# Optimization experiments

Hardware: AMD Instinct MI355X
Metric: run time of the kernel (lower is better)

The kernel has to match this reference:

```python
import jax, jax.numpy as jnp
import numpy as np

DIM = 768
H = 12
D = DIM // H  # head_dim = 64
SCALE = D ** -0.5


def _split_heads(x):
    # [b, n, h*d] -> [b, h, n, d]
    b, n, _ = x.shape
    return x.reshape(b, n, H, D).transpose(0, 2, 1, 3)


def setup_inputs() -> dict:
    key = jax.random.key(0)
    ks = jax.random.split(key, 16)
    B, NQ, NKV = 2, 2048, 2048
    w_init = lambda k: jax.random.normal(k, (DIM, DIM), dtype=jnp.float32) * 0.02
    return {
        "words": jax.random.normal(ks[0], (B, NQ, DIM), dtype=jnp.float32),
        "position_words": jax.random.normal(ks[1], (B, NQ, DIM), dtype=jnp.float32),
        "conscious_words": jax.random.normal(ks[2], (B, NQ, DIM), dtype=jnp.float32),
        "cross_kv": jax.random.normal(ks[3], (B, NKV, DIM), dtype=jnp.float32),
        "position_cross": jax.random.normal(ks[4], (B, NKV, DIM), dtype=jnp.float32),
        "Wq_w": w_init(ks[5]), "Wk_w": w_init(ks[6]), "Wv_w": w_init(ks[7]),
        "Wq_p": w_init(ks[8]), "Wk_p": w_init(ks[9]),
        "Wq_c": w_init(ks[10]), "Wk_c": w_init(ks[11]),
        "latent_k": jax.random.normal(ks[12], (DIM,), dtype=jnp.float32),
        "Wo": w_init(ks[13]),
        "bo": jnp.zeros((DIM,), dtype=jnp.float32),
    }


def reference(words, position_words, conscious_words, cross_kv, position_cross,
              Wq_w, Wk_w, Wv_w, Wq_p, Wk_p, Wq_c, Wk_c, latent_k, Wo, bo):
    # Queries from three sources. Sum of the 9 pairwise QK^T scores equals
    # (sum of Qs) @ (sum of Ks)^T by bilinearity of matmul (same math as source).
    q = _split_heads(words @ Wq_w) + _split_heads(position_words @ Wq_p) \
        + _split_heads(conscious_words @ Wq_c)        # [b,h,nq,d]
    # latent conscious key: same vector for every kv position
    kc = (latent_k @ Wk_c).reshape(H, D)              # [h,d]
    k = _split_heads(cross_kv @ Wk_w) + _split_heads(position_cross @ Wk_p) \
        + kc[None, :, None, :]                        # [b,h,nkv,d]
    v = _split_heads(cross_kv @ Wv_w)                 # [b,h,nkv,d]

    score = jnp.einsum('bhid,bhjd->bhij', q, k) * SCALE  # [b,h,nq,nkv]
    attn = jax.nn.softmax(score, axis=-1)
    out = jnp.einsum('bhij,bhjd->bhid', attn, v)      # [b,h,nq,d]
    b, _, nq, _ = out.shape
    out = out.transpose(0, 2, 1, 3).reshape(b, nq, H * D)
    return out @ Wo + bo
```

## Files before the change

kernel.cpp:

```cpp
#include <hip/hip_runtime.h>
#include <math.h>

#define DIM  768
#define NH   12
#define HD   64
#define NQ   2048
#define NKV  2048
#define QSC_LOG2E 0.18033688011112042f

typedef short bf16x8  __attribute__((ext_vector_type(8)));
typedef float f32x4   __attribute__((ext_vector_type(4)));
typedef float f32x16  __attribute__((ext_vector_type(16)));

__device__ __forceinline__ unsigned short f2bf(float f) {
    unsigned u = __float_as_uint(f);
    unsigned r = (u + 0x7FFFu + ((u >> 16) & 1u)) >> 16;
    return (unsigned short)r;
}

__device__ __forceinline__ unsigned cvtpk_bf16(float a, float b) {
    unsigned r;
    asm("v_cvt_pk_bf16_f32 %0, %1, %2" : "=v"(r) : "v"(a), "v"(b));
    return r;
}

__device__ __forceinline__ void plswap(unsigned& a, unsigned& b) {
    asm("v_permlane32_swap_b32 %0, %1" : "+v"(a), "+v"(b));
}

__device__ __forceinline__ float vexp2f(float x) {
#if __has_builtin(__builtin_amdgcn_exp2f)
    return __builtin_amdgcn_exp2f(x);
#else
    float r;
    asm("v_exp_f32 %0, %1\ns_nop 0" : "=v"(r) : "v"(x));
    return r;
#endif
}

__device__ __forceinline__ void ld_lds16(void* lds, const void* g) {
    __builtin_amdgcn_global_load_lds(
        (const __attribute__((address_space(1))) unsigned int*)g,
        (__attribute__((address_space(3))) unsigned int*)lds, 16, 0, 0);
}

__device__ __forceinline__ f32x16 z16() {
    f32x16 r;
    #pragma unroll
    for (int e = 0; e < 16; ++e) r[e] = 0.f;
    return r;
}

union PB16 { unsigned u[4]; bf16x8 v; };

__global__ __launch_bounds__(256)
void kc2_kernel(const float* __restrict__ latent, const float* __restrict__ Wkc,
                float* __restrict__ kc) {
    __shared__ float red[16][17];
    int tx = threadIdx.x & 15, ty = threadIdx.x >> 4;
    int j = blockIdx.x * 16 + tx;
    float acc = 0.f;
    for (int i = ty * 48; i < ty * 48 + 48; ++i) acc += latent[i] * Wkc[i * DIM + j];
    red[ty][tx] = acc;
    __syncthreads();
    if (ty == 0) {
        float s = 0.f;
        #pragma unroll
        for (int k = 0; k < 16; ++k) s += red[k][tx];
        kc[j] = s;
    }
}

__global__ __launch_bounds__(256)
void convert_acts(const float* __restrict__ s0, const float* __restrict__ s1,
                  const float* __restrict__ s2, const float* __restrict__ s3,
                  const float* __restrict__ s4,
                  unsigned short* __restrict__ dstA, unsigned short* __restrict__ dstB) {
    const float* srcs[5] = {s0, s1, s2, s3, s4};
    int y = blockIdx.y;
    const float* s = srcs[y];
    unsigned short* d = (y < 4) ? (dstA + (size_t)y * 3145728) : dstB;
    size_t i = ((size_t)blockIdx.x * 256 + threadIdx.x) * 4;
    float4 v = *(const float4*)(s + i);
    ushort4 o;
    o.x = f2bf(v.x); o.y = f2bf(v.y); o.z = f2bf(v.z); o.w = f2bf(v.w);
    *(ushort4*)(d + i) = o;
}

__global__ __launch_bounds__(256)
void conv_w(const float* __restrict__ w0, const float* __restrict__ w1,
            const float* __restrict__ w2, const float* __restrict__ w3,
            const float* __restrict__ w4, const float* __restrict__ w5,
            const float* __restrict__ w6, unsigned short* __restrict__ dst) {
    __shared__ float t[32][33];
    const float* Ws[7] = {w0, w1, w2, w3, w4, w5, w6};
    const float* W = Ws[blockIdx.z];
    unsigned short* D = dst + (size_t)blockIdx.z * (768 * 768);
    int r0 = blockIdx.y * 32, c0 = blockIdx.x * 32;
    int tx = threadIdx.x & 31, ty = threadIdx.x >> 5;
    #pragma unroll
    for (int yy = 0; yy < 4; ++yy)
        t[ty * 4 + yy][tx] = W[(size_t)(r0 + ty * 4 + yy) * 768 + c0 + tx];
    __syncthreads();
    #pragma unroll
    for (int yy = 0; yy < 4; ++yy)
        D[(size_t)(c0 + ty * 4 + yy) * 768 + r0 + tx] = f2bf(t[tx][ty * 4 + yy]);
}

template<int NPAIR, int MODE>
__global__ __launch_bounds__(256)
void mfma_gemm(const unsigned short* __restrict__ A0, const unsigned short* __restrict__ B0,
               const unsigned short* __restrict__ A1, const unsigned short* __restrict__ B1,
               const unsigned short* __restrict__ A2, const unsigned short* __restrict__ B2,
               const float* __restrict__ bias, float scale, void* __restrict__ Cout) {
    __shared__ unsigned short As[2][64 * 64];
    __shared__ unsigned short Bs[2][128 * 64];
    const int tid = threadIdx.x;
    const int w = tid >> 6, l = tid & 63, g = l >> 4, r16 = l & 15;

    int o_lin = blockIdx.x + 6 * blockIdx.y;
    int wl = (o_lin & 7) * 48 + (o_lin >> 3);
    int bx = wl % 6, by = wl / 6;
    const int n0 = bx * 128, m0 = by * 64;

    const unsigned short* Alist[3] = {A0, A1, A2};
    const unsigned short* Blist[3] = {B0, B1, B2};

    f32x4 acc[4][2];
    #pragma unroll
    for (int i = 0; i < 4; ++i)
        #pragma unroll
        for (int j = 0; j < 2; ++j) acc[i][j] = (f32x4){0.f, 0.f, 0.f, 0.f};

#define GSTAGE(BUFI, AP, BP, K0) { \
    _Pragma("unroll") \
    for (int is = 0; is < 2; ++is) { \
        int u = is * 256 + tid, r = u >> 3, cc = u & 7; \
        int col = ((cc ^ (r & 7)) << 3); \
        ld_lds16((char*)As[BUFI] + is * 4096 + w * 1024, \
                 (AP) + (size_t)(m0 + r) * 768 + (K0) + col); } \
    _Pragma("unroll") \
    for (int is = 0; is < 4; ++is) { \
        int u = is * 256 + tid, r = u >> 3, cc = u & 7; \
        int col = ((cc ^ (r & 7)) << 3); \
        ld_lds16((char*)Bs[BUFI] + is * 4096 + w * 1024, \
                 (BP) + (size_t)(n0 + r) * 768 + (K0) + col); } }

    const int NSTEPS = NPAIR * 12;
    int pn = 0, kn = 0;
    GSTAGE(0, Alist[0], Blist[0], 0);
    kn = 64; if (kn == 768) { kn = 0; ++pn; }
    __syncthreads();

    #pragma unroll 1
    for (int st = 0; st < NSTEPS; ++st) {
        int cur = st & 1;
        if (st + 1 < NSTEPS) {
            GSTAGE(cur ^ 1, Alist[pn], Blist[pn], kn);
            kn += 64; if (kn == 768) { kn = 0; ++pn; }
        }
        const char* Ab = (const char*)As[cur];
        const char* Bb = (const char*)Bs[cur];
        #pragma unroll
        for (int kk = 0; kk < 2; ++kk) {
            bf16x8 af[4], bf[2];
            #pragma unroll
            for (int i = 0; i < 4; ++i) {
                int row = i * 16 + r16;
                af[i] = *(const bf16x8*)(Ab + row * 128 +
                          ((kk * 64 + g * 16) ^ ((row & 7) << 4)));
            }
            #pragma unroll
            for (int j = 0; j < 2; ++j) {
                int row = w * 32 + j * 16 + r16;
                bf[j] = *(const bf16x8*)(Bb + row * 128 +
                          ((kk * 64 + g * 16) ^ ((row & 7) << 4)));
            }
            #pragma unroll
            for (int i = 0; i < 4; ++i)
                #pragma unroll
                for (int j = 0; j < 2; ++j)
                    acc[i][j] = __builtin_amdgcn_mfma_f32_16x16x32_bf16(
                        af[i], bf[j], acc[i][j], 0, 0, 0);
        }
        __syncthreads();
    }
#undef GSTAGE

    #pragma unroll
    for (int i = 0; i < 4; ++i) {
        #pragma unroll
        for (int j = 0; j < 2; ++j) {
            int col = n0 + w * 32 + j * 16 + r16;
            float bv = ((MODE == 0 && bias) || MODE == 1) ? bias[col] : 0.f;
            #pragma unroll
            for (int rr = 0; rr < 4; ++rr) {
                int row = m0 + i * 16 + g * 4 + rr;
                float v = acc[i][j][rr];
                if (MODE == 2) v *= scale;
                v += bv;
                if (MODE == 1) {
                    ((float*)Cout)[(size_t)row * 768 + col] = v;
                } else if (MODE == 3) {
                    int bb = row >> 11, q = row & 2047;
                    ((unsigned short*)Cout)[(size_t)(bb * 768 + col) * 2048 + q] = f2bf(v);
                } else {
                    ((unsigned short*)Cout)[(size_t)row * 768 + col] = f2bf(v);
                }
            }
        }
    }
}

__global__ __launch_bounds__(256)
void flash2(const unsigned short* __restrict__ Qb,
            const unsigned short* __restrict__ Kb,
            const unsigned short* __restrict__ Vt,
            unsigned short* __restrict__ AO) {
    __shared__ unsigned short KV[2][2][4096];
    const int tid = threadIdx.x;
    const int w = tid >> 6, l = tid & 63, lo = l & 31, hi = l >> 5;

    int o_lin = blockIdx.x + 16 * blockIdx.y;
    int wl = (o_lin & 7) * 48 + (o_lin >> 3);
    int qi = wl & 15, bh = wl >> 4;
    int b = bh / NH, h = bh % NH;
    int q0 = qi * 128;

    bf16x8 qf[4];
    {
        const unsigned short* Qrow =
            Qb + (size_t)(b * NQ + q0 + w * 32 + lo) * DIM + h * HD + hi * 8;
        #pragma unroll
        for (int kc = 0; kc < 4; ++kc) qf[kc] = *(const bf16x8*)(Qrow + kc * 16);
    }

    f32x16 o0 = z16(), o1 = z16();
    float m = -3.0e38f, lsum = 0.f;

    const unsigned short* Kbase = Kb + (size_t)(b * NKV) * DIM + h * HD;
    const unsigned short* Vbase = Vt + ((size_t)b * DIM + h * HD) * NKV;

#define FSTAGE(BUFI, T0) { \
    _Pragma("unroll") \
    for (int is = 0; is < 2; ++is) { \
        int u = is * 256 + tid, r = u >> 3, cc = u & 7; \
        int col = ((cc ^ (r & 7)) << 3); \
        ld_lds16((char*)KV[BUFI][0] + is * 4096 + w * 1024, \
                 Kbase + (size_t)((T0) + r) * 768 + col); \
        ld_lds16((char*)KV[BUFI][1] + is * 4096 + w * 1024, \
                 Vbase + (size_t)r * 2048 + (T0) + col); } }

    FSTAGE(0, 0);
    __syncthreads();

    #pragma unroll 1
    for (int t = 0; t < 32; ++t) {
        int cur = t & 1;
        if (t < 31) FSTAGE(cur ^ 1, (t + 1) * 64);

        const char* Kp = (const char*)KV[cur][0];
        const char* Vp = (const char*)KV[cur][1];

        f32x16 s0 = z16(), s1 = z16();
        #pragma unroll
        for (int kc = 0; kc < 4; ++kc) {
            int r0 = lo, r1 = 32 + lo;
            bf16x8 k0 = *(const bf16x8*)(Kp + r0 * 128 +
                          ((kc * 32 + hi * 16) ^ ((r0 & 7) << 4)));
            bf16x8 k1 = *(const bf16x8*)(Kp + r1 * 128 +
                          ((kc * 32 + hi * 16) ^ ((r1 & 7) << 4)));
            s0 = __builtin_amdgcn_mfma_f32_32x32x16_bf16(k0, qf[kc], s0, 0, 0, 0);
            s1 = __builtin_amdgcn_mfma_f32_32x32x16_bf16(k1, qf[kc], s1, 0, 0, 0);
        }

        float a8[8];
        #pragma unroll
        for (int e = 0; e < 8; ++e)
            a8[e] = fmaxf(fmaxf(s0[e], s0[e + 8]), fmaxf(s1[e], s1[e + 8]));
        #pragma unroll
        for (int e = 0; e < 4; ++e) a8[e] = fmaxf(a8[e], a8[e + 4]);
        float pm = fmaxf(fmaxf(a8[0], a8[1]), fmaxf(a8[2], a8[3]));
        pm = fmaxf(pm, __shfl_xor(pm, 32));

        if (__any(pm > m + 10.f)) {
            float mn = fmaxf(m, pm);
            float sc = vexp2f(m - mn);
            lsum *= sc;
            #pragma unroll
            for (int e = 0; e < 16; ++e) { o0[e] *= sc; o1[e] *= sc; }
            m = mn;
        }

        #pragma unroll
        for (int e = 0; e < 16; ++e) {
            s0[e] = vexp2f(s0[e] - m);
            s1[e] = vexp2f(s1[e] - m);
        }

        float b8[8];
        #pragma unroll
        for (int e = 0; e < 8; ++e)
            b8[e] = (s0[e] + s0[e + 8]) + (s1[e] + s1[e + 8]);
        float rs = ((b8[0] + b8[1]) + (b8[2] + b8[3])) +
                   ((b8[4] + b8[5]) + (b8[6] + b8[7]));
        rs += __shfl_xor(rs, 32);
        lsum += rs;

        PB16 pb[4];
        #pragma unroll
        for (int cc = 0; cc < 2; ++cc) {
            unsigned a0 = cvtpk_bf16(s0[cc * 8 + 0], s0[cc * 8 + 1]);
            unsigned a1 = cvtpk_bf16(s0[cc * 8 + 2], s0[cc * 8 + 3]);
            unsigned b0 = cvtpk_bf16(s0[cc * 8 + 4], s0[cc * 8 + 5]);
            unsigned b1 = cvtpk_bf16(s0[cc * 8 + 6], s0[cc * 8 + 7]);
            plswap(a0, b0);
            plswap(a1, b1);
            pb[cc].u[0] = a0; pb[cc].u[1] = a1; pb[cc].u[2] = b0; pb[cc].u[3] = b1;
            unsigned c0 = cvtpk_bf16(s1[cc * 8 + 0], s1[cc * 8 + 1]);
            unsigned c1 = cvtpk_bf16(s1[cc * 8 + 2], s1[cc * 8 + 3]);
            unsigned d0 = cvtpk_bf16(s1[cc * 8 + 4], s1[cc * 8 + 5]);
            unsigned d1 = cvtpk_bf16(s1[cc * 8 + 6], s1[cc * 8 + 7]);
            plswap(c0, d0);
            plswap(c1, d1);
            pb[2 + cc].u[0] = c0; pb[2 + cc].u[1] = c1;
            pb[2 + cc].u[2] = d0; pb[2 + cc].u[3] = d1;
        }

        #pragma unroll
        for (int c = 0; c < 4; ++c) {
            int r0 = lo, r1 = 32 + lo;
            bf16x8 v0 = *(const bf16x8*)(Vp + r0 * 128 +
                          ((c * 32 + hi * 16) ^ ((r0 & 7) << 4)));
            bf16x8 v1 = *(const bf16x8*)(Vp + r1 * 128 +
                          ((c * 32 + hi * 16) ^ ((r1 & 7) << 4)));
            o0 = __builtin_amdgcn_mfma_f32_32x32x16_bf16(v0, pb[c].v, o0, 0, 0, 0);
            o1 = __builtin_amdgcn_mfma_f32_32x32x16_bf16(v1, pb[c].v, o1, 0, 0, 0);
        }
        __syncthreads();
    }
#undef FSTAGE

    float inv = 1.f / lsum;
    char* eb = (char*)KV + w * 4096;
    #pragma unroll
    for (int r = 0; r < 16; r += 2) {
        int d0 = (r & 3) + 8 * (r >> 2) + 4 * hi;
        *(unsigned*)(eb + lo * 128 + ((2 * d0) ^ ((lo & 7) << 4))) =
            cvtpk_bf16(o0[r] * inv, o0[r + 1] * inv);
        int d1 = 32 + d0;
        *(unsigned*)(eb + lo * 128 + ((2 * d1) ^ ((lo & 7) << 4))) =
            cvtpk_bf16(o1[r] * inv, o1[r + 1] * inv);
    }
    int q2 = l >> 1, h2 = l & 1;
    size_t grow = (size_t)(b * NQ + q0 + w * 32 + q2) * DIM + h * HD + h2 * 32;
    #pragma unroll
    for (int c = 0; c < 4; ++c) {
        uint4 vv = *(const uint4*)(eb + q2 * 128 + ((h2 * 64 + c * 16) ^ ((q2 & 7) << 4)));
        *(uint4*)(AO + grow + c * 8) = vv;
    }
}

extern "C" void kernel_launch(void* const* d_in, const int* in_sizes, int n_in,
                              void* d_out, int out_size, void* d_ws, size_t ws_size,
                              hipStream_t stream) {
    const float* words   = (const float*)d_in[0];
    const float* posw    = (const float*)d_in[1];
    const float* consc   = (const float*)d_in[2];
    const float* cross   = (const float*)d_in[3];
    const float* pcross  = (const float*)d_in[4];
    const float* Wq_w    = (const float*)d_in[5];
    const float* Wk_w    = (const float*)d_in[6];
    const float* Wv_w    = (const float*)d_in[7];
    const float* Wq_p    = (const float*)d_in[8];
    const float* Wk_p    = (const float*)d_in[9];
    const float* Wq_c    = (const float*)d_in[10];
    const float* Wk_c    = (const float*)d_in[11];
    const float* latentk = (const float*)d_in[12];
    const float* Wo      = (const float*)d_in[13];
    const float* bo      = (const float*)d_in[14];

    char* arena = (char*)d_ws;
    const size_t ACTB = 6291456;
    unsigned short* act0 = (unsigned short*)(arena);
    unsigned short* act1 = (unsigned short*)(arena + ACTB);
    unsigned short* act2 = (unsigned short*)(arena + 2 * ACTB);
    unsigned short* act3 = (unsigned short*)(arena + 3 * ACTB);
    unsigned short* wt   = (unsigned short*)(arena + 4 * ACTB);
    const size_t WTE = 768 * 768;
    unsigned short* qb  = (unsigned short*)(arena + 4 * ACTB + 7 * WTE * 2);
    unsigned short* pcb = (unsigned short*)((char*)qb + ACTB);
    float* kcv          = (float*)((char*)pcb + ACTB);

    unsigned short* kb = act1;
    unsigned short* vt = act2;
    unsigned short* ao = act0;

    convert_acts<<<dim3(3072, 5), dim3(256), 0, stream>>>(
        words, posw, consc, cross, pcross, act0, pcb);
    conv_w<<<dim3(24, 24, 7), dim3(256), 0, stream>>>(
        Wq_w, Wq_p, Wq_c, Wk_w, Wk_p, Wv_w, Wo, wt);
    kc2_kernel<<<dim3(48), dim3(256), 0, stream>>>(latentk, Wk_c, kcv);

    mfma_gemm<3, 2><<<dim3(6, 64), dim3(256), 0, stream>>>(
        act0, wt + 0 * WTE, act1, wt + 1 * WTE, act2, wt + 2 * WTE,
        nullptr, QSC_LOG2E, qb);
    mfma_gemm<1, 3><<<dim3(6, 64), dim3(256), 0, stream>>>(
        act3, wt + 5 * WTE, nullptr, nullptr, nullptr, nullptr,
        nullptr, 1.f, vt);
    mfma_gemm<2, 0><<<dim3(6, 64), dim3(256), 0, stream>>>(
        act3, wt + 3 * WTE, pcb, wt + 4 * WTE, nullptr, nullptr,
        kcv, 1.f, kb);
    flash2<<<dim3(16, 24), dim3(256), 0, stream>>>(qb, kb, vt, ao);
    mfma_gemm<1, 1><<<dim3(6, 64), dim3(256), 0, stream>>>(
        ao, wt + 6 * WTE, nullptr, nullptr, nullptr, nullptr,
        bo, 1.f, (float*)d_out);
}
```

Baseline: 160.0 us.

## Fuse fp32 conversion into QKV GEMM, merge launches, split-KV flash with combine

Drops the separate activation-conversion kernel: the QKV GEMM now loads fp32 activations directly and converts them to bf16 while staging into LDS. The Q, V and K projections are merged into one launch with XCD-aware block mapping, and the weight-transpose and latent-key kernels are merged into one prep kernel. Flash attention is split four ways over the KV length for more parallelism, writing unnormalized partials plus max and sum that a new combine kernel merges. MFMA sections get s_setprio hints. The changes cut launch count and activation traffic, but they add partial-buffer traffic, an extra combine pass and register pressure from the fp32 A loads.

```diff
diff --git a/kernel.cpp b/kernel.cpp
--- a/kernel.cpp
+++ b/kernel.cpp
@@ -16,6 +16,9 @@
     unsigned u = __float_as_uint(f);
     unsigned r = (u + 0x7FFFu + ((u >> 16) & 1u)) >> 16;
     return (unsigned short)r;
+}
+__device__ __forceinline__ float bf2f(unsigned short u) {
+    return __uint_as_float(((unsigned)u) << 16);
 }
 
 __device__ __forceinline__ unsigned cvtpk_bf16(float a, float b) {
@@ -54,111 +57,218 @@
 union PB16 { unsigned u[4]; bf16x8 v; };
 
 __global__ __launch_bounds__(256)
-void kc2_kernel(const float* __restrict__ latent, const float* __restrict__ Wkc,
-                float* __restrict__ kc) {
-    __shared__ float red[16][17];
-    int tx = threadIdx.x & 15, ty = threadIdx.x >> 4;
-    int j = blockIdx.x * 16 + tx;
-    float acc = 0.f;
-    for (int i = ty * 48; i < ty * 48 + 48; ++i) acc += latent[i] * Wkc[i * DIM + j];
-    red[ty][tx] = acc;
-    __syncthreads();
-    if (ty == 0) {
-        float s = 0.f;
-        #pragma unroll
-        for (int k = 0; k < 16; ++k) s += red[k][tx];
-        kc[j] = s;
-    }
-}
+void prep_kernel(const float* __restrict__ w0, const float* __restrict__ w1,
+                 const float* __restrict__ w2, const float* __restrict__ w3,
+                 const float* __restrict__ w4, const float* __restrict__ w5,
+                 const float* __restrict__ w6, unsigned short* __restrict__ wt,
+                 const float* __restrict__ latent, const float* __restrict__ Wkc,
+                 float* __restrict__ kc) {
+    __shared__ float t[32][33];
+    int bid = blockIdx.x;
+    if (bid < 4032) {
+        int iz = bid / 576, rem = bid - iz * 576;
+        int iy = rem / 24, ix = rem - iy * 24;
+        const float* Ws[7] = {w0, w1, w2, w3, w4, w5, w6};
+        const float* W = Ws[iz];
+        unsigned short* D = wt + (size_t)iz * (768 * 768);
+        int r0 = iy * 32, c0 = ix * 32;
+        int tx = threadIdx.x & 31, ty = threadIdx.x >> 5;
+        #pragma unroll
+        for (int yy = 0; yy < 4; ++yy)
+            t[ty * 4 + yy][tx] = W[(size_t)(r0 + ty * 4 + yy) * 768 + c0 + tx];
+        __syncthreads();
+        #pragma unroll
+        for (int yy = 0; yy < 4; ++yy)
+            D[(size_t)(c0 + ty * 4 + yy) * 768 + r0 + tx] = f2bf(t[tx][ty * 4 + yy]);
+    } else {
+        int jb = bid - 4032;
+        float (&red)[16][17] = *reinterpret_cast<float(*)[16][17]>(&t[0][0]);
+        int tx = threadIdx.x & 15, ty = threadIdx.x >> 4;
+        int j = jb * 16 + tx;
+        float acc = 0.f;
+        for (int i = ty * 48; i < ty * 48 + 48; ++i)
+            acc += latent[i] * Wkc[i * DIM + j];
+        red[ty][tx] = acc;
+        __syncthreads();
+        if (ty == 0) {
+            float s = 0.f;
+            #pragma unroll
+            for (int k = 0; k < 16; ++k) s += red[k][tx];
+            kc[j] = s;
+        }
+    }
+}
+
+struct QCfg {
+    const float* A0; const float* A1; const float* A2;
+    const unsigned short* B0; const unsigned short* B1; const unsigned short* B2;
+    const float* bias; float scale; void* out; int npair; int mode;
+};
 
 __global__ __launch_bounds__(256)
-void convert_acts(const float* __restrict__ s0, const float* __restrict__ s1,
-                  const float* __restrict__ s2, const float* __restrict__ s3,
-                  const float* __restrict__ s4,
-                  unsigned short* __restrict__ dstA, unsigned short* __restrict__ dstB) {
-    const float* srcs[5] = {s0, s1, s2, s3, s4};
-    int y = blockIdx.y;
-    const float* s = srcs[y];
-    unsigned short* d = (y < 4) ? (dstA + (size_t)y * 3145728) : dstB;
-    size_t i = ((size_t)blockIdx.x * 256 + threadIdx.x) * 4;
-    float4 v = *(const float4*)(s + i);
-    ushort4 o;
-    o.x = f2bf(v.x); o.y = f2bf(v.y); o.z = f2bf(v.z); o.w = f2bf(v.w);
-    *(ushort4*)(d + i) = o;
-}
-
-__global__ __launch_bounds__(256)
-void conv_w(const float* __restrict__ w0, const float* __restrict__ w1,
-            const float* __restrict__ w2, const float* __restrict__ w3,
-            const float* __restrict__ w4, const float* __restrict__ w5,
-            const float* __restrict__ w6, unsigned short* __restrict__ dst) {
-    __shared__ float t[32][33];
-    const float* Ws[7] = {w0, w1, w2, w3, w4, w5, w6};
-    const float* W = Ws[blockIdx.z];
-    unsigned short* D = dst + (size_t)blockIdx.z * (768 * 768);
-    int r0 = blockIdx.y * 32, c0 = blockIdx.x * 32;
-    int tx = threadIdx.x & 31, ty = threadIdx.x >> 5;
-    #pragma unroll
-    for (int yy = 0; yy < 4; ++yy)
-        t[ty * 4 + yy][tx] = W[(size_t)(r0 + ty * 4 + yy) * 768 + c0 + tx];
-    __syncthreads();
-    #pragma unroll
-    for (int yy = 0; yy < 4; ++yy)
-        D[(size_t)(c0 + ty * 4 + yy) * 768 + r0 + tx] = f2bf(t[tx][ty * 4 + yy]);
-}
-
-template<int NPAIR, int MODE>
-__global__ __launch_bounds__(256)
-void mfma_gemm(const unsigned short* __restrict__ A0, const unsigned short* __restrict__ B0,
-               const unsigned short* __restrict__ A1, const unsigned short* __restrict__ B1,
-               const unsigned short* __restrict__ A2, const unsigned short* __restrict__ B2,
-               const float* __restrict__ bias, float scale, void* __restrict__ Cout) {
+void gemm_qvk(QCfg c0, QCfg c1, QCfg c2) {
     __shared__ unsigned short As[2][64 * 64];
     __shared__ unsigned short Bs[2][128 * 64];
     const int tid = threadIdx.x;
     const int w = tid >> 6, l = tid & 63, g = l >> 4, r16 = l & 15;
 
-    int o_lin = blockIdx.x + 6 * blockIdx.y;
+    int p = blockIdx.x;
+    int xcd = p & 7, s = p >> 3;
+    int bx = s % 6, gg = s / 6;
+    int gidx = gg * 8 + xcd;
+    int by = gidx & 63, z = gidx >> 6;
+    const int n0 = bx * 128, m0 = by * 64;
+
+    QCfg c = (z == 0) ? c0 : (z == 1) ? c1 : c2;
+    const float* Alist[3] = {c.A0, c.A1, c.A2};
+    const unsigned short* Blist[3] = {c.B0, c.B1, c.B2};
+
+    const int ar = tid >> 2, ac = (tid & 3) * 16;
+    const int aswz = (ar & 7) << 4;
+    float4 av0, av1, av2, av3;
+
+    f32x4 acc[4][2];
+    #pragma unroll
+    for (int i = 0; i < 4; ++i)
+        #pragma unroll
+        for (int j = 0; j < 2; ++j) acc[i][j] = (f32x4){0.f, 0.f, 0.f, 0.f};
+
+#define ALOAD(AP, K0) { \
+    const float* _ap = (AP) + (size_t)(m0 + ar) * 768 + (K0) + ac; \
+    av0 = *(const float4*)_ap;       av1 = *(const float4*)(_ap + 4); \
+    av2 = *(const float4*)(_ap + 8); av3 = *(const float4*)(_ap + 12); }
+
+#define AWRITE(BUFI) { \
+    uint4 u0_, u1_; \
+    u0_.x = cvtpk_bf16(av0.x, av0.y); u0_.y = cvtpk_bf16(av0.z, av0.w); \
+    u0_.z = cvtpk_bf16(av1.x, av1.y); u0_.w = cvtpk_bf16(av1.z, av1.w); \
+    u1_.x = cvtpk_bf16(av2.x, av2.y); u1_.y = cvtpk_bf16(av2.z, av2.w); \
+    u1_.z = cvtpk_bf16(av3.x, av3.y); u1_.w = cvtpk_bf16(av3.z, av3.w); \
+    *(uint4*)((char*)As[BUFI] + ar * 128 + ((2 * ac) ^ aswz)) = u0_; \
+    *(uint4*)((char*)As[BUFI] + ar * 128 + ((2 * ac + 16) ^ aswz)) = u1_; }
+
+#define BSTAGE(BUFI, BP, K0) { _Pragma("unroll") \
+    for (int is = 0; is < 4; ++is) { \
+        int u = is * 256 + tid, r = u >> 3, cc = u & 7; \
+        int col = ((cc ^ (r & 7)) << 3); \
+        ld_lds16((char*)Bs[BUFI] + is * 4096 + w * 1024, \
+                 (BP) + (size_t)(n0 + r) * 768 + (K0) + col); } }
+
+    const int NSTEPS = c.npair * 12;
+    int pn = 0, kn = 0;
+    ALOAD(Alist[0], 0);
+    BSTAGE(0, Blist[0], 0);
+    AWRITE(0);
+    kn = 64;
+    __syncthreads();
+
+    #pragma unroll 1
+    for (int st = 0; st < NSTEPS; ++st) {
+        int cur = st & 1;
+        bool pre = (st + 1 < NSTEPS);
+        if (pre) {
+            ALOAD(Alist[pn], kn);
+            BSTAGE(cur ^ 1, Blist[pn], kn);
+        }
+        const char* Ab = (const char*)As[cur];
+        const char* Bb = (const char*)Bs[cur];
+        #pragma unroll
+        for (int kk = 0; kk < 2; ++kk) {
+            bf16x8 af[4], bf[2];
+            #pragma unroll
+            for (int i = 0; i < 4; ++i) {
+                int row = i * 16 + r16;
+                af[i] = *(const bf16x8*)(Ab + row * 128 +
+                          ((kk * 64 + g * 16) ^ ((row & 7) << 4)));
+            }
+            #pragma unroll
+            for (int j = 0; j < 2; ++j) {
+                int row = w * 32 + j * 16 + r16;
+                bf[j] = *(const bf16x8*)(Bb + row * 128 +
+                          ((kk * 64 + g * 16) ^ ((row & 7) << 4)));
+            }
+            #pragma unroll
+            for (int i = 0; i < 4; ++i)
+                #pragma unroll
+                for (int j = 0; j < 2; ++j)
+                    acc[i][j] = __builtin_amdgcn_mfma_f32_16x16x32_bf16(
+                        af[i], bf[j], acc[i][j], 0, 0, 0);
+        }
+        if (pre) {
+            AWRITE(cur ^ 1);
+            kn += 64; if (kn == 768) { kn = 0; ++pn; }
+        }
+        __syncthreads();
+    }
+#undef ALOAD
+#undef AWRITE
+#undef BSTAGE
+
+    const int mode = c.mode;
+    #pragma unroll
+    for (int i = 0; i < 4; ++i) {
+        #pragma unroll
+        for (int j = 0; j < 2; ++j) {
+            int col = n0 + w * 32 + j * 16 + r16;
+            float bv = (mode == 0 && c.bias) ? c.bias[col] : 0.f;
+            #pragma unroll
+            for (int rr = 0; rr < 4; ++rr) {
+                int row = m0 + i * 16 + g * 4 + rr;
+                float v = acc[i][j][rr];
+                if (mode == 2) v *= c.scale;
+                v += bv;
+                if (mode == 3) {
+                    int bb = row >> 11, q = row & 2047;
+                    ((unsigned short*)c.out)[(size_t)(bb * 768 + col) * 2048 + q] = f2bf(v);
+                } else {
+                    ((unsigned short*)c.out)[(size_t)row * 768 + col] = f2bf(v);
+                }
+            }
+        }
+    }
+}
+
+__global__ __launch_bounds__(256)
+void gemm_out(const unsigned short* __restrict__ A,
+              const unsigned short* __restrict__ B,
+              const float* __restrict__ bias, float* __restrict__ Cout) {
+    __shared__ unsigned short As[2][64 * 64];
+    __shared__ unsigned short Bs[2][128 * 64];
+    const int tid = threadIdx.x;
+    const int w = tid >> 6, l = tid & 63, g = l >> 4, r16 = l & 15;
+
+    int o_lin = blockIdx.x;
     int wl = (o_lin & 7) * 48 + (o_lin >> 3);
     int bx = wl % 6, by = wl / 6;
     const int n0 = bx * 128, m0 = by * 64;
 
-    const unsigned short* Alist[3] = {A0, A1, A2};
-    const unsigned short* Blist[3] = {B0, B1, B2};
-
     f32x4 acc[4][2];
     #pragma unroll
     for (int i = 0; i < 4; ++i)
         #pragma unroll
         for (int j = 0; j < 2; ++j) acc[i][j] = (f32x4){0.f, 0.f, 0.f, 0.f};
 
-#define GSTAGE(BUFI, AP, BP, K0) { \
+#define GSTAGE(BUFI, K0) { \
     _Pragma("unroll") \
     for (int is = 0; is < 2; ++is) { \
         int u = is * 256 + tid, r = u >> 3, cc = u & 7; \
         int col = ((cc ^ (r & 7)) << 3); \
         ld_lds16((char*)As[BUFI] + is * 4096 + w * 1024, \
-                 (AP) + (size_t)(m0 + r) * 768 + (K0) + col); } \
+                 A + (size_t)(m0 + r) * 768 + (K0) + col); } \
     _Pragma("unroll") \
     for (int is = 0; is < 4; ++is) { \
         int u = is * 256 + tid, r = u >> 3, cc = u & 7; \
         int col = ((cc ^ (r & 7)) << 3); \
         ld_lds16((char*)Bs[BUFI] + is * 4096 + w * 1024, \
-                 (BP) + (size_t)(n0 + r) * 768 + (K0) + col); } }
-
-    const int NSTEPS = NPAIR * 12;
-    int pn = 0, kn = 0;
-    GSTAGE(0, Alist[0], Blist[0], 0);
-    kn = 64; if (kn == 768) { kn = 0; ++pn; }
+                 B + (size_t)(n0 + r) * 768 + (K0) + col); } }
+
+    GSTAGE(0, 0);
     __syncthreads();
 
     #pragma unroll 1
-    for (int st = 0; st < NSTEPS; ++st) {
+    for (int st = 0; st < 12; ++st) {
         int cur = st & 1;
-        if (st + 1 < NSTEPS) {
-            GSTAGE(cur ^ 1, Alist[pn], Blist[pn], kn);
-            kn += 64; if (kn == 768) { kn = 0; ++pn; }
-        }
+        if (st + 1 < 12) GSTAGE(cur ^ 1, (st + 1) * 64);
         const char* Ab = (const char*)As[cur];
         const char* Bb = (const char*)Bs[cur];
         #pragma unroll
@@ -192,21 +302,11 @@
         #pragma unroll
         for (int j = 0; j < 2; ++j) {
             int col = n0 + w * 32 + j * 16 + r16;
-            float bv = ((MODE == 0 && bias) || MODE == 1) ? bias[col] : 0.f;
+            float bv = bias[col];
             #pragma unroll
             for (int rr = 0; rr < 4; ++rr) {
                 int row = m0 + i * 16 + g * 4 + rr;
-                float v = acc[i][j][rr];
-                if (MODE == 2) v *= scale;
-                v += bv;
-                if (MODE == 1) {
-                    ((float*)Cout)[(size_t)row * 768 + col] = v;
-                } else if (MODE == 3) {
-                    int bb = row >> 11, q = row & 2047;
-                    ((unsigned short*)Cout)[(size_t)(bb * 768 + col) * 2048 + q] = f2bf(v);
-                } else {
-                    ((unsigned short*)Cout)[(size_t)row * 768 + col] = f2bf(v);
-                }
+                Cout[(size_t)row * 768 + col] = acc[i][j][rr] + bv;
             }
         }
     }
@@ -216,16 +316,21 @@
 void flash2(const unsigned short* __restrict__ Qb,
             const unsigned short* __restrict__ Kb,
             const unsigned short* __restrict__ Vt,
-            unsigned short* __restrict__ AO) {
+            unsigned short* __restrict__ P0, unsigned short* __restrict__ P1,
+            unsigned short* __restrict__ P2, unsigned short* __restrict__ P3,
+            float2* __restrict__ ML) {
     __shared__ unsigned short KV[2][2][4096];
     const int tid = threadIdx.x;
     const int w = tid >> 6, l = tid & 63, lo = l & 31, hi = l >> 5;
 
-    int o_lin = blockIdx.x + 16 * blockIdx.y;
-    int wl = (o_lin & 7) * 48 + (o_lin >> 3);
-    int qi = wl & 15, bh = wl >> 4;
+    int p = blockIdx.x + 64 * blockIdx.y;
+    int xcd = p & 7, s = p >> 3;
+    int gg = s >> 6, inner = s & 63;
+    int bh = gg * 8 + xcd;
+    int qi = inner >> 2, part = inner & 3;
     int b = bh / NH, h = bh % NH;
     int q0 = qi * 128;
+    int kvbase = part * 512;
 
     bf16x8 qf[4];
     {
@@ -251,18 +356,19 @@
         ld_lds16((char*)KV[BUFI][1] + is * 4096 + w * 1024, \
                  Vbase + (size_t)r * 2048 + (T0) + col); } }
 
-    FSTAGE(0, 0);
+    FSTAGE(0, kvbase);
     __syncthreads();
 
     #pragma unroll 1
-    for (int t = 0; t < 32; ++t) {
+    for (int t = 0; t < 8; ++t) {
         int cur = t & 1;
-        if (t < 31) FSTAGE(cur ^ 1, (t + 1) * 64);
+        if (t < 7) FSTAGE(cur ^ 1, kvbase + (t + 1) * 64);
 
         const char* Kp = (const char*)KV[cur][0];
         const char* Vp = (const char*)KV[cur][1];
 
         f32x16 s0 = z16(), s1 = z16();
+        __builtin_amdgcn_s_setprio(1);
         #pragma unroll
         for (int kc = 0; kc < 4; ++kc) {
             int r0 = lo, r1 = 32 + lo;
@@ -273,14 +379,14 @@
             s0 = __builtin_amdgcn_mfma_f32_32x32x16_bf16(k0, qf[kc], s0, 0, 0, 0);
             s1 = __builtin_amdgcn_mfma_f32_32x32x16_bf16(k1, qf[kc], s1, 0, 0, 0);
         }
+        __builtin_amdgcn_s_setprio(0);
 
         float a8[8];
         #pragma unroll
         for (int e = 0; e < 8; ++e)
-            a8[e] = fmaxf(fmaxf(s0[e], s0[e + 8]), fmaxf(s1[e], s1[e + 8]));
-        #pragma unroll
-        for (int e = 0; e < 4; ++e) a8[e] = fmaxf(a8[e], a8[e + 4]);
-        float pm = fmaxf(fmaxf(a8[0], a8[1]), fmaxf(a8[2], a8[3]));
+            a8[e] = fmaxf(fmaxf(fmaxf(s0[e], s0[e + 8]), s1[e]), s1[e + 8]);
+        float pm = fmaxf(fmaxf(fmaxf(fmaxf(a8[0], a8[1]), fmaxf(a8[2], a8[3])),
+                               fmaxf(fmaxf(a8[4], a8[5]), fmaxf(a8[6], a8[7]))), -3.0e38f);
         pm = fmaxf(pm, __shfl_xor(pm, 32));
 
         if (__any(pm > m + 10.f)) {
@@ -327,6 +433,7 @@
             pb[2 + cc].u[2] = d0; pb[2 + cc].u[3] = d1;
         }
 
+        __builtin_amdgcn_s_setprio(1);
         #pragma unroll
         for (int c = 0; c < 4; ++c) {
             int r0 = lo, r1 = 32 + lo;
@@ -337,27 +444,81 @@
             o0 = __builtin_amdgcn_mfma_f32_32x32x16_bf16(v0, pb[c].v, o0, 0, 0, 0);
             o1 = __builtin_amdgcn_mfma_f32_32x32x16_bf16(v1, pb[c].v, o1, 0, 0, 0);
         }
+        __builtin_amdgcn_s_setprio(0);
         __syncthreads();
     }
 #undef FSTAGE
 
-    float inv = 1.f / lsum;
-    char* eb = (char*)KV + w * 4096;
-    #pragma unroll
-    for (int r = 0; r < 16; r += 2) {
-        int d0 = (r & 3) + 8 * (r >> 2) + 4 * hi;
-        *(unsigned*)(eb + lo * 128 + ((2 * d0) ^ ((lo & 7) << 4))) =
-            cvtpk_bf16(o0[r] * inv, o0[r + 1] * inv);
-        int d1 = 32 + d0;
-        *(unsigned*)(eb + lo * 128 + ((2 * d1) ^ ((lo & 7) << 4))) =
-            cvtpk_bf16(o1[r] * inv, o1[r + 1] * inv);
-    }
-    int q2 = l >> 1, h2 = l & 1;
-    size_t grow = (size_t)(b * NQ + q0 + w * 32 + q2) * DIM + h * HD + h2 * 32;
+    unsigned short* Pp = (part == 0) ? P0 : (part == 1) ? P1 : (part == 2) ? P2 : P3;
+    const int q = q0 + w * 32 + lo;
+    unsigned short* Op = Pp + ((size_t)bh * 2048 + q) * 64;
+    #pragma unroll
+    for (int grp = 0; grp < 4; ++grp) {
+        int r0 = grp * 4;
+        int d0 = grp * 8 + 4 * hi;
+        uint2 v0, v1;
+        v0.x = cvtpk_bf16(o0[r0 + 0], o0[r0 + 1]);
+        v0.y = cvtpk_bf16(o0[r0 + 2], o0[r0 + 3]);
+        *(uint2*)(Op + d0) = v0;
+        v1.x = cvtpk_bf16(o1[r0 + 0], o1[r0 + 1]);
+        v1.y = cvtpk_bf16(o1[r0 + 2], o1[r0 + 3]);
+        *(uint2*)(Op + 32 + d0) = v1;
+    }
+    if (hi == 0)
+        ML[(size_t)(part * 24 + bh) * 2048 + q] = make_float2(m, lsum);
+}
+
+__global__ __launch_bounds__(256)
+void combine4(const unsigned short* __restrict__ P0, const unsigned short* __restrict__ P1,
+              const unsigned short* __restrict__ P2, const unsigned short* __restrict__ P3,
+              const float2* __restrict__ ML, unsigned short* __restrict__ AO) {
+    int bh = blockIdx.y;
+    int idx = blockIdx.x * 256 + threadIdx.x;
+    int q = idx >> 1, dh = (idx & 1) * 32;
+
+    float2 u0 = ML[(size_t)(0 * 24 + bh) * 2048 + q];
+    float2 u1 = ML[(size_t)(1 * 24 + bh) * 2048 + q];
+    float2 u2 = ML[(size_t)(2 * 24 + bh) * 2048 + q];
+    float2 u3 = ML[(size_t)(3 * 24 + bh) * 2048 + q];
+    float M = fmaxf(fmaxf(u0.x, u1.x), fmaxf(u2.x, u3.x));
+    float w0 = vexp2f(u0.x - M), w1 = vexp2f(u1.x - M);
+    float w2 = vexp2f(u2.x - M), w3 = vexp2f(u3.x - M);
+    float inv = 1.f / (w0 * u0.y + w1 * u1.y + w2 * u2.y + w3 * u3.y);
+    w0 *= inv; w1 *= inv; w2 *= inv; w3 *= inv;
+
+    size_t off = ((size_t)bh * 2048 + q) * 64 + dh;
+    float acc[32];
+    #pragma unroll
+    for (int e = 0; e < 32; ++e) acc[e] = 0.f;
+    const unsigned short* Ps[4] = {P0, P1, P2, P3};
+    float ws[4] = {w0, w1, w2, w3};
+    #pragma unroll
+    for (int pp = 0; pp < 4; ++pp) {
+        const unsigned short* src = Ps[pp] + off;
+        float wv = ws[pp];
+        #pragma unroll
+        for (int c = 0; c < 4; ++c) {
+            ushort4 hh2;
+            uint4 vv = *(const uint4*)(src + c * 8);
+            unsigned uu[4] = {vv.x, vv.y, vv.z, vv.w};
+            #pragma unroll
+            for (int e = 0; e < 4; ++e) {
+                acc[c * 8 + e * 2 + 0] += wv * bf2f((unsigned short)(uu[e] & 0xFFFF));
+                acc[c * 8 + e * 2 + 1] += wv * bf2f((unsigned short)(uu[e] >> 16));
+            }
+            (void)hh2;
+        }
+    }
+    int b = bh / NH, h = bh % NH;
+    unsigned short* dst = AO + ((size_t)(b * 2048 + q)) * DIM + h * HD + dh;
     #pragma unroll
     for (int c = 0; c < 4; ++c) {
-        uint4 vv = *(const uint4*)(eb + q2 * 128 + ((h2 * 64 + c * 16) ^ ((q2 & 7) << 4)));
-        *(uint4*)(AO + grow + c * 8) = vv;
+        uint4 ov;
+        ov.x = cvtpk_bf16(acc[c * 8 + 0], acc[c * 8 + 1]);
+        ov.y = cvtpk_bf16(acc[c * 8 + 2], acc[c * 8 + 3]);
+        ov.z = cvtpk_bf16(acc[c * 8 + 4], acc[c * 8 + 5]);
+        ov.w = cvtpk_bf16(acc[c * 8 + 6], acc[c * 8 + 7]);
+        *(uint4*)(dst + c * 8) = ov;
     }
 }
 
@@ -381,38 +542,35 @@
     const float* bo      = (const float*)d_in[14];
 
     char* arena = (char*)d_ws;
-    const size_t ACTB = 6291456;
-    unsigned short* act0 = (unsigned short*)(arena);
-    unsigned short* act1 = (unsigned short*)(arena + ACTB);
-    unsigned short* act2 = (unsigned short*)(arena + 2 * ACTB);
-    unsigned short* act3 = (unsigned short*)(arena + 3 * ACTB);
-    unsigned short* wt   = (unsigned short*)(arena + 4 * ACTB);
     const size_t WTE = 768 * 768;
-    unsigned short* qb  = (unsigned short*)(arena + 4 * ACTB + 7 * WTE * 2);
-    unsigned short* pcb = (unsigned short*)((char*)qb + ACTB);
-    float* kcv          = (float*)((char*)pcb + ACTB);
-
-    unsigned short* kb = act1;
-    unsigned short* vt = act2;
-    unsigned short* ao = act0;
-
-    convert_acts<<<dim3(3072, 5), dim3(256), 0, stream>>>(
-        words, posw, consc, cross, pcross, act0, pcb);
-    conv_w<<<dim3(24, 24, 7), dim3(256), 0, stream>>>(
-        Wq_w, Wq_p, Wq_c, Wk_w, Wk_p, Wv_w, Wo, wt);
-    kc2_kernel<<<dim3(48), dim3(256), 0, stream>>>(latentk, Wk_c, kcv);
-
-    mfma_gemm<3, 2><<<dim3(6, 64), dim3(256), 0, stream>>>(
-        act0, wt + 0 * WTE, act1, wt + 1 * WTE, act2, wt + 2 * WTE,
-        nullptr, QSC_LOG2E, qb);
-    mfma_gemm<1, 3><<<dim3(6, 64), dim3(256), 0, stream>>>(
-        act3, wt + 5 * WTE, nullptr, nullptr, nullptr, nullptr,
-        nullptr, 1.f, vt);
-    mfma_gemm<2, 0><<<dim3(6, 64), dim3(256), 0, stream>>>(
-        act3, wt + 3 * WTE, pcb, wt + 4 * WTE, nullptr, nullptr,
-        kcv, 1.f, kb);
-    flash2<<<dim3(16, 24), dim3(256), 0, stream>>>(qb, kb, vt, ao);
-    mfma_gemm<1, 1><<<dim3(6, 64), dim3(256), 0, stream>>>(
-        ao, wt + 6 * WTE, nullptr, nullptr, nullptr, nullptr,
-        bo, 1.f, (float*)d_out);
-}
+    unsigned short* WT = (unsigned short*)(arena);
+    unsigned short* QB = (unsigned short*)(arena + 8257536);
+    unsigned short* VT = (unsigned short*)(arena + 14548992);
+    unsigned short* KB = (unsigned short*)(arena + 20840448);
+    unsigned short* P0 = (unsigned short*)(arena + 27131904);
+    unsigned short* P1 = (unsigned short*)(arena + 33423360);
+    unsigned short* P2 = (unsigned short*)(arena + 39714816);
+    unsigned short* P3 = (unsigned short*)(arena);
+    float2* ML         = (float2*)(arena + 46006272);
+    float* KCV         = (float*)(arena + 47579136);
+
+    prep_kernel<<<dim3(4080), dim3(256), 0, stream>>>(
+        Wq_w, Wq_p, Wq_c, Wk_w, Wk_p, Wv_w, Wo, WT, latentk, Wk_c, KCV);
+
+    QCfg cq = { words, posw, consc,
+                WT + 0 * WTE, WT + 1 * WTE, WT + 2 * WTE,
+                nullptr, QSC_LOG2E, QB, 3, 2 };
+    QCfg cv = { cross, nullptr, nullptr,
+                WT + 5 * WTE, nullptr, nullptr,
+                nullptr, 1.f, VT, 1, 3 };
+    QCfg ck = { cross, pcross, nullptr,
+                WT + 3 * WTE, WT + 4 * WTE, nullptr,
+                KCV, 1.f, KB, 2, 0 };
+    gemm_qvk<<<dim3(1152), dim3(256), 0, stream>>>(cq, cv, ck);
+
+    flash2<<<dim3(64, 24), dim3(256), 0, stream>>>(QB, KB, VT, P0, P1, P2, P3, ML);
+
+    combine4<<<dim3(16, 24), dim3(256), 0, stream>>>(P0, P1, P2, P3, ML, QB);
+
+    gemm_out<<<dim3(384), dim3(256), 0, stream>>>(QB, WT + 6 * WTE, bo, (float*)d_out);
+}
```

Result: faster. 140.0 us (-12.5%).
